# Kernel optimization log

Hardware: AMD Instinct MI355X
Metric: run time of the kernel (lower is better)

## Reference

```python
import jax, jax.numpy as jnp
import numpy as np

HEADS = 4
NDECAY = 4


def setup_inputs() -> dict:
    key = jax.random.key(0)
    ks = jax.random.split(key, 6)
    B, C, T = 4, 192, 2048
    s = 1.0 / np.sqrt(C)
    return {
        "x": jax.random.normal(ks[0], (B, C, T), dtype=jnp.float32),
        "Wq": jax.random.normal(ks[1], (C, C), dtype=jnp.float32) * s,
        "bq": jnp.zeros((C,), dtype=jnp.float32),
        "Wk": jax.random.normal(ks[2], (C, C), dtype=jnp.float32) * s,
        "bk": jnp.zeros((C,), dtype=jnp.float32),
        "Wc": jax.random.normal(ks[3], (C, C), dtype=jnp.float32) * s,
        "bc": jnp.zeros((C,), dtype=jnp.float32),
        "Wd": jax.random.normal(ks[4], (C, HEADS * NDECAY), dtype=jnp.float32) * s,
        "bd": jnp.zeros((HEADS * NDECAY,), dtype=jnp.float32),
        "Wp": jax.random.normal(ks[5], (C, C), dtype=jnp.float32) * s,
        "bp": jnp.zeros((C,), dtype=jnp.float32),
    }


def reference(x, Wq, bq, Wk, bk, Wc, bc, Wd, bd, Wp, bp):
    B, C, T = x.shape
    heads, ndecay = HEADS, NDECAY
    hd = C // heads
    xt = jnp.transpose(x, (0, 2, 1))  # (B, T, C)

    def split_heads(y):  # (B, T, D) -> (B, heads, D//heads, T)
        return jnp.transpose(y, (0, 2, 1)).reshape(B, heads, -1, T)

    queries = split_heads(xt @ Wq + bq)   # (B, h, hd, T)
    keys = split_heads(xt @ Wk + bk)      # (B, h, hd, T)
    content = split_heads(xt @ Wc + bc)   # (B, h, hd, T)

    # dots[b,h,t,s] = <keys[...,t], queries[...,s]> / sqrt(hd)
    dots = jnp.einsum('bhct,bhcs->bhts', keys, queries) / jnp.sqrt(
        jnp.asarray(hd, x.dtype))

    # learned decay bias
    decay_q = split_heads(xt @ Wd + bd)                 # (B, h, ndecay, T)
    decay_q = jax.nn.sigmoid(decay_q) / 2
    delta = (jnp.arange(T, dtype=x.dtype)[:, None]
             - jnp.arange(T, dtype=x.dtype)[None, :])   # (T, T)
    decays = jnp.arange(1, ndecay + 1, dtype=x.dtype)
    decay_kernel = -decays.reshape(-1, 1, 1) * jnp.abs(delta) / jnp.sqrt(
        jnp.asarray(ndecay, x.dtype))                   # (ndecay, T, T)
    dots = dots + jnp.einsum('fts,bhfs->bhts', decay_kernel, decay_q)

    # mask diagonal
    idx = jnp.arange(T)
    dots = dots.at[..., idx, idx].set(-100)

    weights = jax.nn.softmax(dots, axis=2)              # softmax over t (keys)
    result = jnp.einsum('bhts,bhct->bhcs', weights, content).reshape(B, C, T)

    out = jnp.transpose(result, (0, 2, 1)) @ Wp + bp + xt  # (B, T, C)
    return jnp.transpose(out, (0, 2, 1))                    # (B, C, T)
```

## Files before the change

kernel.cpp:

```cpp
#include <hip/hip_runtime.h>

typedef __attribute__((ext_vector_type(8))) short short8;
typedef __attribute__((ext_vector_type(4))) float f32x4;

constexpr int Bn = 4, Cn = 192, Tn = 2048, Hn = 4, HD = 48;
constexpr float LOG2E = 1.4426950408889634f;
constexpr float QK_SCALE2 = 0.14433756729740643f * 1.4426950408889634f;
constexpr float NEG100_LOG2 = -100.0f * 1.4426950408889634f;

__device__ inline unsigned short f2bf(float f) {
  unsigned int u = __builtin_bit_cast(unsigned int, f);
  return (unsigned short)((u + 0x7FFFu + ((u >> 16) & 1u)) >> 16);
}
__device__ inline float bf2f(unsigned short h) {
  unsigned int u = ((unsigned int)h) << 16;
  return __builtin_bit_cast(float, u);
}
__device__ inline f32x4 mfma16(short8 a, short8 b, f32x4 c) {
  return __builtin_amdgcn_mfma_f32_16x16x32_bf16(a, b, c, 0, 0, 0);
}
__device__ inline unsigned int cvtpk(float lo, float hi) {
  unsigned int r;
  asm("v_cvt_pk_bf16_f32 %0, %1, %2" : "=v"(r) : "v"(lo), "v"(hi));
  return r;
}

__global__ __launch_bounds__(256) void transpose_x(const float* __restrict__ x,
                                                   short* __restrict__ xt) {
  __shared__ short tile[32][40];
  int t0 = blockIdx.x * 32, c0 = blockIdx.y * 32, b = blockIdx.z;
  int tid = threadIdx.x;
  int row = tid >> 3, q = tid & 7;
  float4 v = *(const float4*)(x + ((size_t)(b * Cn + c0 + row)) * Tn + t0 + q * 4);
  tile[row][q * 4 + 0] = (short)f2bf(v.x);
  tile[row][q * 4 + 1] = (short)f2bf(v.y);
  tile[row][q * 4 + 2] = (short)f2bf(v.z);
  tile[row][q * 4 + 3] = (short)f2bf(v.w);
  __syncthreads();
  ushort4 pk;
  pk.x = (unsigned short)tile[q * 4 + 0][row];
  pk.y = (unsigned short)tile[q * 4 + 1][row];
  pk.z = (unsigned short)tile[q * 4 + 2][row];
  pk.w = (unsigned short)tile[q * 4 + 3][row];
  *(ushort4*)(xt + ((size_t)(b * Tn + t0 + row)) * Cn + c0 + q * 4) = pk;
}

__global__ void prep_w(const float* __restrict__ Wq, const float* __restrict__ Wk,
                       const float* __restrict__ Wc, const float* __restrict__ Wp,
                       short* __restrict__ WT) {
  int n = blockIdx.x, j = blockIdx.y, k = threadIdx.x;
  const float* W = (j == 0) ? Wq : (j == 1) ? Wk : (j == 2) ? Wc : Wp;
  WT[((size_t)j * Cn + n) * Cn + k] = (short)f2bf(W[(size_t)k * Cn + n]);
}

__global__ __launch_bounds__(256) void gemm_qkv(const short* __restrict__ WT,
                                                const float* __restrict__ bq,
                                                const float* __restrict__ bk,
                                                const float* __restrict__ bc,
                                                const short* __restrict__ Bsrc,
                                                short* __restrict__ Qt,
                                                short* __restrict__ Kt,
                                                short* __restrict__ Vc) {
  constexpr int LDK = 200;
  __shared__ short As[64 * LDK];
  __shared__ short Bs[128 * LDK];
  int tt = blockIdx.x, nt = blockIdx.y, b = blockIdx.z;
  int j = nt / 3;
  int ln0 = (nt - j * 3) * 64;
  int n0g = nt * 64;
  int t0 = tt * 128;
  const float* bias = (j == 0) ? bq : (j == 1) ? bk : bc;
  int tid = threadIdx.x, w = tid >> 6, l = tid & 63;
  int g16 = l >> 4, c16 = l & 15;

  for (int idx = tid; idx < 4608; idx += 256) {
    if (idx < 1536) {
      int row = idx / 24, ch = idx % 24;
      *(float4*)(&As[row * LDK + ch * 8]) =
          *(const float4*)(WT + ((size_t)(n0g + row)) * Cn + ch * 8);
    } else {
      int jj = idx - 1536;
      int row = jj / 24, ch = jj % 24;
      *(float4*)(&Bs[row * LDK + ch * 8]) =
          *(const float4*)(Bsrc + ((size_t)(b * Tn + t0 + row)) * Cn + ch * 8);
    }
  }
  __syncthreads();

  f32x4 acc[4][2];
#pragma unroll
  for (int m = 0; m < 4; ++m)
#pragma unroll
    for (int n = 0; n < 2; ++n) acc[m][n] = (f32x4){0.f, 0.f, 0.f, 0.f};

#pragma unroll
  for (int kk = 0; kk < 6; ++kk) {
    short8 af[4], bf[2];
#pragma unroll
    for (int m = 0; m < 4; ++m)
      af[m] = *(const short8*)(&As[(m * 16 + c16) * LDK + kk * 32 + g16 * 8]);
#pragma unroll
    for (int n = 0; n < 2; ++n)
      bf[n] = *(const short8*)(&Bs[(w * 32 + n * 16 + c16) * LDK + kk * 32 + g16 * 8]);
#pragma unroll
    for (int m = 0; m < 4; ++m)
#pragma unroll
      for (int n = 0; n < 2; ++n) acc[m][n] = mfma16(af[m], bf[n], acc[m][n]);
  }

#pragma unroll
  for (int m = 0; m < 4; ++m)
#pragma unroll
    for (int n = 0; n < 2; ++n) {
      int nrow = ln0 + m * 16 + g16 * 4;
      int tcol = t0 + w * 32 + n * 16 + c16;
      if (j == 2) {
#pragma unroll
        for (int r = 0; r < 4; ++r)
          Vc[((size_t)(b * Cn + nrow + r)) * Tn + tcol] =
              (short)f2bf(acc[m][n][r] + bias[nrow + r]);
      } else {
        short* O = j ? Kt : Qt;
        ushort4 pk;
        pk.x = f2bf(acc[m][n][0] + bias[nrow + 0]);
        pk.y = f2bf(acc[m][n][1] + bias[nrow + 1]);
        pk.z = f2bf(acc[m][n][2] + bias[nrow + 2]);
        pk.w = f2bf(acc[m][n][3] + bias[nrow + 3]);
        *(ushort4*)(O + ((size_t)(b * Tn + tcol)) * Cn + nrow) = pk;
      }
    }
}

__global__ __launch_bounds__(256) void decay_g(const short* __restrict__ xt,
                                               const float* __restrict__ Wd,
                                               const float* __restrict__ bd,
                                               float* __restrict__ gout) {
  int idx = blockIdx.x * 256 + threadIdx.x;
  int kq = idx & 7;
  int t = (idx >> 3) & 2047;
  int b = idx >> 14;
  const short* xr = xt + ((size_t)(b * Tn + t)) * Cn + kq * 24;
  const float* wr = Wd + kq * 24 * 16;
  float d[16];
#pragma unroll
  for (int n = 0; n < 16; ++n) d[n] = 0.f;
#pragma unroll
  for (int k = 0; k < 24; k += 8) {
    short8 xv8 = *(const short8*)(xr + k);
#pragma unroll
    for (int jj = 0; jj < 8; ++jj) {
      float xv = bf2f((unsigned short)xv8[jj]);
      const float* wrow = wr + (k + jj) * 16;
#pragma unroll
      for (int n = 0; n < 16; ++n) d[n] = fmaf(xv, wrow[n], d[n]);
    }
  }
#pragma unroll
  for (int n = 0; n < 16; ++n) {
    d[n] += __shfl_xor(d[n], 1);
    d[n] += __shfl_xor(d[n], 2);
    d[n] += __shfl_xor(d[n], 4);
  }
  if (kq == 0) {
#pragma unroll
    for (int h = 0; h < 4; ++h) {
      float gsum = 0.f;
#pragma unroll
      for (int f = 0; f < 4; ++f) {
        float s = 1.f / (1.f + __expf(-(d[h * 4 + f] + bd[h * 4 + f])));
        gsum += (float)(f + 1) * s;
      }
      gout[((size_t)(b * 4 + h)) * Tn + t] = 0.25f * gsum;
    }
  }
}

__global__ __launch_bounds__(256, 4) void attn(const short* __restrict__ Qt,
                                               const short* __restrict__ Kt,
                                               const short* __restrict__ Vc,
                                               const float* __restrict__ gbuf,
                                               unsigned short* __restrict__ Pacc,
                                               float* __restrict__ Plsum,
                                               int kchunk) {
  __shared__ short Kb[2][64][64];
  __shared__ short Vb[2][48][64];
  __shared__ short Pl[4][16][64];
  const int s0 = blockIdx.x * 64;
  const int bh = blockIdx.y;
  const int b = bh >> 2, h = bh & 3;
  const int ks = blockIdx.z;
  const int tid = threadIdx.x, w = tid >> 6, l = tid & 63;
  const int g16 = l >> 4, c16 = l & 15;
  const int sx = c16 & 7;
  const int tstart = ks * kchunk, tend = tstart + kchunk;

  const short* Kbase = Kt + (size_t)b * Tn * Cn + h * HD;
  const short* Vbase = Vc + ((size_t)(b * Cn + h * HD)) * Tn;

  float4 z4;
  z4.x = z4.y = z4.z = z4.w = 0.f;
  {
    int bufz = tid >> 7, r = (tid & 127) >> 1, chp = 6 + (tid & 1);
    *(float4*)(&Kb[bufz][r][(chp ^ (r & 7)) * 8]) = z4;
  }
  for (int idx = tid; idx < 384; idx += 256) {
    int row = idx / 6, ch = idx % 6;
    *(float4*)(&Kb[0][row][(ch ^ (row & 7)) * 8]) =
        *(const float4*)(Qt + ((size_t)(b * Tn + s0 + row)) * Cn + h * HD + ch * 8);
  }
  __syncthreads();
  short8 qf[2];
  {
    int qr = w * 16 + c16;
    qf[0] = *(const short8*)(&Kb[0][qr][(g16 ^ sx) * 8]);
    qf[1] = *(const short8*)(&Kb[0][qr][((4 + g16) ^ sx) * 8]);
  }
  __syncthreads();

  for (int idx = tid; idx < 768; idx += 256) {
    if (idx < 384) {
      int row = idx / 6, ch = idx % 6;
      *(float4*)(&Kb[0][row][(ch ^ (row & 7)) * 8]) =
          *(const float4*)(Kbase + ((size_t)(tstart + row)) * Cn + ch * 8);
    } else {
      int jj = idx - 384, row = jj >> 3, ch = jj & 7;
      *(float4*)(&Vb[0][row][(ch ^ (row & 7)) * 8]) =
          *(const float4*)(Vbase + (size_t)row * Tn + tstart + ch * 8);
    }
  }
  __syncthreads();

  const int kr0 = tid / 6, kc0 = tid % 6;
  const bool r1K = tid < 128;
  const int r1row = r1K ? (tid + 256) / 6 : ((tid - 128) >> 3);
  const int r1ch = r1K ? (tid + 256) % 6 : ((tid - 128) & 7);
  const int vr2 = (tid + 128) >> 3, vc2 = (tid + 128) & 7;
  const int dK0 = kr0 * 64 + ((kc0 ^ (kr0 & 7)) * 8);
  const int dR1 = r1row * 64 + ((r1ch ^ (r1row & 7)) * 8);
  const int dV2 = vr2 * 64 + ((vc2 ^ (vr2 & 7)) * 8);

  const int s_lane = s0 + w * 16 + c16;
  const float g2 = gbuf[((size_t)(b * 4 + h)) * Tn + s_lane] * LOG2E;
  const float g16x = g2 * 16.0f;
  const float rb1 = g2, rb2 = g2 * 2.0f, rb3 = g2 * 3.0f;
  float base = g2 * (float)(tstart + g16 * 4 - s_lane);
  const float binc = g2 * 64.0f;
  float lsum = 0.f;
  f32x4 acc[3];
#pragma unroll
  for (int cs = 0; cs < 3; ++cs) acc[cs] = (f32x4){0.f, 0.f, 0.f, 0.f};

  int buf = 0;
  for (int t0 = tstart; t0 < tend; t0 += 64) {
    const int tn = t0 + 64;
    const bool hn = tn < tend;
    float4 r0, r1, r2;
    if (hn) {
      r0 = *(const float4*)(Kbase + (size_t)(tn + kr0) * Cn + kc0 * 8);
      r1 = r1K ? *(const float4*)(Kbase + (size_t)(tn + r1row) * Cn + r1ch * 8)
               : *(const float4*)(Vbase + (size_t)r1row * Tn + tn + r1ch * 8);
      r2 = *(const float4*)(Vbase + (size_t)vr2 * Tn + tn + vc2 * 8);
    }
    const short* KbP = &Kb[buf][0][0];
    const short* VbP = &Vb[buf][0][0];

    f32x4 sacc[4];
#pragma unroll
    for (int m = 0; m < 4; ++m) sacc[m] = (f32x4){0.f, 0.f, 0.f, 0.f};
    __builtin_amdgcn_s_setprio(1);
#pragma unroll
    for (int kk = 0; kk < 2; ++kk)
#pragma unroll
      for (int m = 0; m < 4; ++m) {
        short8 af = *(const short8*)(KbP + (m * 16 + c16) * 64 + (((kk * 4 + g16) ^ sx) * 8));
        sacc[m] = mfma16(af, qf[kk], sacc[m]);
      }
    __builtin_amdgcn_s_setprio(0);

    if (t0 > s0) {
      float nbm = -base;
#pragma unroll
      for (int m = 0; m < 4; ++m) {
        float e0 = __builtin_amdgcn_exp2f(fmaf(sacc[m][0], QK_SCALE2, nbm));
        float e1 = __builtin_amdgcn_exp2f(fmaf(sacc[m][1], QK_SCALE2, nbm) - rb1);
        float e2 = __builtin_amdgcn_exp2f(fmaf(sacc[m][2], QK_SCALE2, nbm) - rb2);
        float e3 = __builtin_amdgcn_exp2f(fmaf(sacc[m][3], QK_SCALE2, nbm) - rb3);
        lsum += (e0 + e1) + (e2 + e3);
        unsigned long long u64v =
            ((unsigned long long)cvtpk(e2, e3) << 32) | (unsigned long long)cvtpk(e0, e1);
        *(unsigned long long*)(&Pl[w][c16][(((2 * m + (g16 >> 1)) ^ sx) * 8) + (g16 & 1) * 4]) =
            u64v;
        nbm -= g16x;
      }
    } else if (t0 < s0) {
      float pbm = base;
#pragma unroll
      for (int m = 0; m < 4; ++m) {
        float e0 = __builtin_amdgcn_exp2f(fmaf(sacc[m][0], QK_SCALE2, pbm));
        float e1 = __builtin_amdgcn_exp2f(fmaf(sacc[m][1], QK_SCALE2, pbm) + rb1);
        float e2 = __builtin_amdgcn_exp2f(fmaf(sacc[m][2], QK_SCALE2, pbm) + rb2);
        float e3 = __builtin_amdgcn_exp2f(fmaf(sacc[m][3], QK_SCALE2, pbm) + rb3);
        lsum += (e0 + e1) + (e2 + e3);
        unsigned long long u64v =
            ((unsigned long long)cvtpk(e2, e3) << 32) | (unsigned long long)cvtpk(e0, e1);
        *(unsigned long long*)(&Pl[w][c16][(((2 * m + (g16 >> 1)) ^ sx) * 8) + (g16 & 1) * 4]) =
            u64v;
        pbm += g16x;
      }
    } else {
      const float fbd = (float)(t0 + g16 * 4 - s_lane);
#pragma unroll
      for (int m = 0; m < 4; ++m) {
        float e[4];
#pragma unroll
        for (int r = 0; r < 4; ++r) {
          float d = fbd + (float)(16 * m + r);
          float ad = fabsf(d);
          float v = fmaf(-g2, ad, sacc[m][r] * QK_SCALE2);
          v = (ad < 0.5f) ? NEG100_LOG2 : v;
          e[r] = __builtin_amdgcn_exp2f(v);
        }
        lsum += (e[0] + e[1]) + (e[2] + e[3]);
        unsigned long long u64v = ((unsigned long long)cvtpk(e[2], e[3]) << 32) |
                                  (unsigned long long)cvtpk(e[0], e[1]);
        *(unsigned long long*)(&Pl[w][c16][(((2 * m + (g16 >> 1)) ^ sx) * 8) + (g16 & 1) * 4]) =
            u64v;
      }
    }
    base += binc;
    asm volatile("s_waitcnt lgkmcnt(0)" ::: "memory");

    __builtin_amdgcn_s_setprio(1);
#pragma unroll
    for (int kk = 0; kk < 2; ++kk) {
      short8 pf = *(const short8*)(&Pl[w][c16][((kk * 4 + g16) ^ sx) * 8]);
#pragma unroll
      for (int cs = 0; cs < 3; ++cs) {
        short8 vf = *(const short8*)(VbP + (cs * 16 + c16) * 64 + (((kk * 4 + g16) ^ sx) * 8));
        acc[cs] = mfma16(vf, pf, acc[cs]);
      }
    }
    __builtin_amdgcn_s_setprio(0);
    __syncthreads();
    if (hn) {
      short* KbN = &Kb[buf ^ 1][0][0];
      short* VbN = &Vb[buf ^ 1][0][0];
      *(float4*)(KbN + dK0) = r0;
      if (r1K)
        *(float4*)(KbN + dR1) = r1;
      else
        *(float4*)(VbN + dR1) = r1;
      *(float4*)(VbN + dV2) = r2;
    }
    __syncthreads();
    buf ^= 1;
  }

  float lsum2 = lsum + __shfl_xor(lsum, 16);
  lsum2 += __shfl_xor(lsum2, 32);
  if (g16 == 0) Plsum[((size_t)(ks * 16 + bh)) * Tn + s_lane] = lsum2;

  unsigned int* Ob = (unsigned int*)&Kb[0][0][0];
  const int orow = w * 16 + c16;
#pragma unroll
  for (int cs = 0; cs < 3; ++cs) {
    Ob[orow * 24 + cs * 8 + g16 * 2 + 0] = cvtpk(acc[cs][0], acc[cs][1]);
    Ob[orow * 24 + cs * 8 + g16 * 2 + 1] = cvtpk(acc[cs][2], acc[cs][3]);
  }
  __syncthreads();
  float4* dst = (float4*)(Pacc + (((size_t)(ks * 16 + bh)) * Tn + s0) * 48);
  const float4* src = (const float4*)Ob;
  dst[tid] = src[tid];
  if (tid < 128) dst[tid + 256] = src[tid + 256];
}

__global__ __launch_bounds__(256) void combine(const unsigned short* __restrict__ Pacc,
                                               const float* __restrict__ Plsum,
                                               short* __restrict__ Rt, int KS) {
  int idx = blockIdx.x * 256 + threadIdx.x;
  int c4 = idx % 48;
  int rest = idx / 48;
  int s = rest & 2047;
  int b = rest >> 11;
  int c = c4 * 4;
  int h = c / 48;
  int cc = c - h * 48;
  size_t qb = ((size_t)(b * 4 + h)) * Tn + s;
  float a0 = 0.f, a1 = 0.f, a2 = 0.f, a3 = 0.f, lt = 0.f;
  for (int ks = 0; ks < KS; ++ks) {
    ushort4 v = *(const ushort4*)(Pacc + ((size_t)ks * 16 * Tn + qb) * 48 + cc);
    a0 += bf2f(v.x);
    a1 += bf2f(v.y);
    a2 += bf2f(v.z);
    a3 += bf2f(v.w);
    lt += Plsum[(size_t)ks * 16 * Tn + qb];
  }
  float inv = 1.f / lt;
  ushort4 pk;
  pk.x = f2bf(a0 * inv);
  pk.y = f2bf(a1 * inv);
  pk.z = f2bf(a2 * inv);
  pk.w = f2bf(a3 * inv);
  *(ushort4*)(Rt + ((size_t)(b * Tn + s)) * Cn + c) = pk;
}

__global__ __launch_bounds__(256) void gemm_out(const short* __restrict__ Awt,
                                                const float* __restrict__ bias,
                                                const short* __restrict__ Bsrc,
                                                float* __restrict__ O,
                                                const float* __restrict__ Xres) {
  constexpr int LDK = 200;
  __shared__ short As[64 * LDK];
  __shared__ short Bs[128 * LDK];
  int tt = blockIdx.x, nt = blockIdx.y, b = blockIdx.z;
  int n0 = nt * 64, t0 = tt * 128;
  int tid = threadIdx.x, w = tid >> 6, l = tid & 63;
  int g16 = l >> 4, c16 = l & 15;

  for (int idx = tid; idx < 4608; idx += 256) {
    if (idx < 1536) {
      int row = idx / 24, ch = idx % 24;
      *(float4*)(&As[row * LDK + ch * 8]) =
          *(const float4*)(Awt + ((size_t)(n0 + row)) * Cn + ch * 8);
    } else {
      int j = idx - 1536;
      int row = j / 24, ch = j % 24;
      *(float4*)(&Bs[row * LDK + ch * 8]) =
          *(const float4*)(Bsrc + ((size_t)(b * Tn + t0 + row)) * Cn + ch * 8);
    }
  }
  __syncthreads();

  f32x4 acc[4][2];
#pragma unroll
  for (int m = 0; m < 4; ++m)
#pragma unroll
    for (int n = 0; n < 2; ++n) acc[m][n] = (f32x4){0.f, 0.f, 0.f, 0.f};

#pragma unroll
  for (int kk = 0; kk < 6; ++kk) {
    short8 af[4], bf[2];
#pragma unroll
    for (int m = 0; m < 4; ++m)
      af[m] = *(const short8*)(&As[(m * 16 + c16) * LDK + kk * 32 + g16 * 8]);
#pragma unroll
    for (int n = 0; n < 2; ++n)
      bf[n] = *(const short8*)(&Bs[(w * 32 + n * 16 + c16) * LDK + kk * 32 + g16 * 8]);
#pragma unroll
    for (int m = 0; m < 4; ++m)
#pragma unroll
      for (int n = 0; n < 2; ++n) acc[m][n] = mfma16(af[m], bf[n], acc[m][n]);
  }

#pragma unroll
  for (int m = 0; m < 4; ++m)
#pragma unroll
    for (int n = 0; n < 2; ++n) {
      int nrow = n0 + m * 16 + g16 * 4;
      int tcol = t0 + w * 32 + n * 16 + c16;
#pragma unroll
      for (int r = 0; r < 4; ++r) {
        size_t i = ((size_t)(b * Cn + nrow + r)) * Tn + tcol;
        O[i] = acc[m][n][r] + bias[nrow + r] + Xres[i];
      }
    }
}

extern "C" void kernel_launch(void* const* d_in, const int* in_sizes, int n_in,
                              void* d_out, int out_size, void* d_ws, size_t ws_size,
                              hipStream_t stream) {
  const float* x = (const float*)d_in[0];
  const float* Wq = (const float*)d_in[1];
  const float* bq = (const float*)d_in[2];
  const float* Wk = (const float*)d_in[3];
  const float* bk = (const float*)d_in[4];
  const float* Wc = (const float*)d_in[5];
  const float* bc = (const float*)d_in[6];
  const float* Wd = (const float*)d_in[7];
  const float* bd = (const float*)d_in[8];
  const float* Wp = (const float*)d_in[9];
  const float* bp = (const float*)d_in[10];
  float* out = (float*)d_out;

  char* ws = (char*)d_ws;
  const size_t SZ = (size_t)Bn * Tn * Cn * sizeof(short);
  short* XTbf = (short*)(ws);
  short* Qt = (short*)(ws + SZ);
  short* Kt = (short*)(ws + 2 * SZ);
  short* Vc = (short*)(ws + 3 * SZ);
  short* Rt = (short*)(ws + 4 * SZ);
  short* WT = (short*)(ws + 5 * SZ);
  float* gbuf = (float*)(ws + 5 * SZ + 294912);
  char* pbase = ws + 5 * SZ + 294912 + 131072;

  const size_t base = 5 * SZ + 294912 + 131072;
  const size_t perks = (size_t)16 * Tn * 48 * 2 + (size_t)16 * Tn * 4;
  int KS = 2;
  if (ws_size && base + 2 * perks > ws_size) KS = 1;
  unsigned short* Pacc = (unsigned short*)pbase;
  float* Plsum = (float*)(pbase + (size_t)KS * 16 * Tn * 48 * 2);

  transpose_x<<<dim3(Tn / 32, Cn / 32, Bn), 256, 0, stream>>>(x, XTbf);
  prep_w<<<dim3(Cn, 4), Cn, 0, stream>>>(Wq, Wk, Wc, Wp, WT);
  gemm_qkv<<<dim3(16, 9, Bn), 256, 0, stream>>>(WT, bq, bk, bc, XTbf, Qt, Kt, Vc);
  decay_g<<<dim3(256), 256, 0, stream>>>(XTbf, Wd, bd, gbuf);
  attn<<<dim3(Tn / 64, Bn * Hn, KS), 256, 0, stream>>>(Qt, Kt, Vc, gbuf, Pacc, Plsum,
                                                       Tn / KS);
  combine<<<dim3(Bn * Tn * 48 / 256), 256, 0, stream>>>(Pacc, Plsum, Rt, KS);
  gemm_out<<<dim3(16, 3, Bn), 256, 0, stream>>>(WT + 3 * 36864, bp, Rt, out, x);
}
```

Before: 82.61 us.

## Double attention query tile per block to share K/V tiles across eight waves

The attention kernel now handles 128 query positions per block with 512 threads (eight waves) instead of 64 queries with four waves. Each K/V tile staged in shared memory is reused by twice as many queries, which halves global K/V load traffic and staging per query. The diagonal-tile test uses a per-wave-group reference, and the load and store index mappings are rewritten for 512 threads. In exchange the grid has half as many blocks. The launch bound of 512 threads with 4 blocks per CU also tightens the register budget, which could cause spills.

```diff
diff --git a/kernel.cpp b/kernel.cpp
--- a/kernel.cpp
+++ b/kernel.cpp
@@ -175,7 +175,7 @@
   }
 }
 
-__global__ __launch_bounds__(256, 4) void attn(const short* __restrict__ Qt,
+__global__ __launch_bounds__(512, 4) void attn(const short* __restrict__ Qt,
                                                const short* __restrict__ Kt,
                                                const short* __restrict__ Vc,
                                                const float* __restrict__ gbuf,
@@ -184,8 +184,8 @@
                                                int kchunk) {
   __shared__ short Kb[2][64][64];
   __shared__ short Vb[2][48][64];
-  __shared__ short Pl[4][16][64];
-  const int s0 = blockIdx.x * 64;
+  __shared__ short Pl[8][16][64];
+  const int s0 = blockIdx.x * 128;
   const int bh = blockIdx.y;
   const int b = bh >> 2, h = bh & 3;
   const int ks = blockIdx.z;
@@ -199,25 +199,25 @@
 
   float4 z4;
   z4.x = z4.y = z4.z = z4.w = 0.f;
-  {
-    int bufz = tid >> 7, r = (tid & 127) >> 1, chp = 6 + (tid & 1);
+  if (tid < 256) {
+    int bufz = tid >> 7, r = (tid >> 1) & 63, chp = 6 + (tid & 1);
     *(float4*)(&Kb[bufz][r][(chp ^ (r & 7)) * 8]) = z4;
   }
-  for (int idx = tid; idx < 384; idx += 256) {
+  for (int idx = tid; idx < 768; idx += 512) {
     int row = idx / 6, ch = idx % 6;
-    *(float4*)(&Kb[0][row][(ch ^ (row & 7)) * 8]) =
+    *(float4*)(&Kb[row >> 6][row & 63][(ch ^ (row & 7)) * 8]) =
         *(const float4*)(Qt + ((size_t)(b * Tn + s0 + row)) * Cn + h * HD + ch * 8);
   }
   __syncthreads();
   short8 qf[2];
   {
-    int qr = w * 16 + c16;
-    qf[0] = *(const short8*)(&Kb[0][qr][(g16 ^ sx) * 8]);
-    qf[1] = *(const short8*)(&Kb[0][qr][((4 + g16) ^ sx) * 8]);
-  }
-  __syncthreads();
-
-  for (int idx = tid; idx < 768; idx += 256) {
+    int qr = (w & 3) * 16 + c16, qb_ = w >> 2;
+    qf[0] = *(const short8*)(&Kb[qb_][qr][(g16 ^ sx) * 8]);
+    qf[1] = *(const short8*)(&Kb[qb_][qr][((4 + g16) ^ sx) * 8]);
+  }
+  __syncthreads();
+
+  for (int idx = tid; idx < 768; idx += 512) {
     if (idx < 384) {
       int row = idx / 6, ch = idx % 6;
       *(float4*)(&Kb[0][row][(ch ^ (row & 7)) * 8]) =
@@ -230,16 +230,16 @@
   }
   __syncthreads();
 
-  const int kr0 = tid / 6, kc0 = tid % 6;
-  const bool r1K = tid < 128;
-  const int r1row = r1K ? (tid + 256) / 6 : ((tid - 128) >> 3);
-  const int r1ch = r1K ? (tid + 256) % 6 : ((tid - 128) & 7);
-  const int vr2 = (tid + 128) >> 3, vc2 = (tid + 128) & 7;
-  const int dK0 = kr0 * 64 + ((kc0 ^ (kr0 & 7)) * 8);
-  const int dR1 = r1row * 64 + ((r1ch ^ (r1row & 7)) * 8);
-  const int dV2 = vr2 * 64 + ((vc2 ^ (vr2 & 7)) * 8);
+  const bool aIsK = tid < 384;
+  const int arow = aIsK ? tid / 6 : ((tid - 384) >> 3);
+  const int ach = aIsK ? tid % 6 : ((tid - 384) & 7);
+  const int dA = arow * 64 + ((ach ^ (arow & 7)) * 8);
+  const bool hasB = tid < 256;
+  const int brow = (128 + tid) >> 3, bch = (128 + tid) & 7;
+  const int dB = brow * 64 + ((bch ^ (brow & 7)) * 8);
 
   const int s_lane = s0 + w * 16 + c16;
+  const int sref = s0 + ((w >> 2) << 6);
   const float g2 = gbuf[((size_t)(b * 4 + h)) * Tn + s_lane] * LOG2E;
   const float g16x = g2 * 16.0f;
   const float rb1 = g2, rb2 = g2 * 2.0f, rb3 = g2 * 3.0f;
@@ -254,12 +254,11 @@
   for (int t0 = tstart; t0 < tend; t0 += 64) {
     const int tn = t0 + 64;
     const bool hn = tn < tend;
-    float4 r0, r1, r2;
+    float4 r0, r1;
     if (hn) {
-      r0 = *(const float4*)(Kbase + (size_t)(tn + kr0) * Cn + kc0 * 8);
-      r1 = r1K ? *(const float4*)(Kbase + (size_t)(tn + r1row) * Cn + r1ch * 8)
-               : *(const float4*)(Vbase + (size_t)r1row * Tn + tn + r1ch * 8);
-      r2 = *(const float4*)(Vbase + (size_t)vr2 * Tn + tn + vc2 * 8);
+      r0 = aIsK ? *(const float4*)(Kbase + (size_t)(tn + arow) * Cn + ach * 8)
+                : *(const float4*)(Vbase + (size_t)arow * Tn + tn + ach * 8);
+      if (hasB) r1 = *(const float4*)(Vbase + (size_t)brow * Tn + tn + bch * 8);
     }
     const short* KbP = &Kb[buf][0][0];
     const short* VbP = &Vb[buf][0][0];
@@ -277,7 +276,7 @@
       }
     __builtin_amdgcn_s_setprio(0);
 
-    if (t0 > s0) {
+    if (t0 > sref) {
       float nbm = -base;
 #pragma unroll
       for (int m = 0; m < 4; ++m) {
@@ -292,7 +291,7 @@
             u64v;
         nbm -= g16x;
       }
-    } else if (t0 < s0) {
+    } else if (t0 < sref) {
       float pbm = base;
 #pragma unroll
       for (int m = 0; m < 4; ++m) {
@@ -345,12 +344,11 @@
     if (hn) {
       short* KbN = &Kb[buf ^ 1][0][0];
       short* VbN = &Vb[buf ^ 1][0][0];
-      *(float4*)(KbN + dK0) = r0;
-      if (r1K)
-        *(float4*)(KbN + dR1) = r1;
+      if (aIsK)
+        *(float4*)(KbN + dA) = r0;
       else
-        *(float4*)(VbN + dR1) = r1;
-      *(float4*)(VbN + dV2) = r2;
+        *(float4*)(VbN + dA) = r0;
+      if (hasB) *(float4*)(VbN + dB) = r1;
     }
     __syncthreads();
     buf ^= 1;
@@ -371,7 +369,7 @@
   float4* dst = (float4*)(Pacc + (((size_t)(ks * 16 + bh)) * Tn + s0) * 48);
   const float4* src = (const float4*)Ob;
   dst[tid] = src[tid];
-  if (tid < 128) dst[tid + 256] = src[tid + 256];
+  if (tid < 256) dst[tid + 512] = src[tid + 512];
 }
 
 __global__ __launch_bounds__(256) void combine(const unsigned short* __restrict__ Pacc,
@@ -504,8 +502,8 @@
   prep_w<<<dim3(Cn, 4), Cn, 0, stream>>>(Wq, Wk, Wc, Wp, WT);
   gemm_qkv<<<dim3(16, 9, Bn), 256, 0, stream>>>(WT, bq, bk, bc, XTbf, Qt, Kt, Vc);
   decay_g<<<dim3(256), 256, 0, stream>>>(XTbf, Wd, bd, gbuf);
-  attn<<<dim3(Tn / 64, Bn * Hn, KS), 256, 0, stream>>>(Qt, Kt, Vc, gbuf, Pacc, Plsum,
-                                                       Tn / KS);
+  attn<<<dim3(Tn / 128, Bn * Hn, KS), 512, 0, stream>>>(Qt, Kt, Vc, gbuf, Pacc, Plsum,
+                                                        Tn / KS);
   combine<<<dim3(Bn * Tn * 48 / 256), 256, 0, stream>>>(Pacc, Plsum, Rt, KS);
   gemm_out<<<dim3(16, 3, Bn), 256, 0, stream>>>(WT + 3 * 36864, bp, Rt, out, x);
 }
```

Result: no change. 81.56 us (-1.3%).
